# Performance work log

Measured on AMD Instinct MI355X. Metric: run time of the kernel, lower is better.

## Reference

```python
import jax, jax.numpy as jnp
import numpy as np

N_NODES = 50000
N_EDGES = 800000
D = 64        # in_channels == out_channels
EDGE_DIM = 32
H = 8         # num_heads
HD = D // H   # head_dim


def _layer_norm(x, g, b, eps=1e-5):
    m = jnp.mean(x, axis=-1, keepdims=True)
    v = jnp.mean((x - m) ** 2, axis=-1, keepdims=True)
    return (x - m) * jax.lax.rsqrt(v + eps) * g + b


def setup_inputs() -> dict:
    key = jax.random.key(0)
    ks = jax.random.split(key, 20)
    s = 0.05
    inp = {
        'x': jax.random.normal(ks[0], (N_NODES, D), jnp.float32),
        'edge_index': jax.random.randint(ks[1], (2, N_EDGES), 0, N_NODES, dtype=jnp.int64),
        'edge_attr': jax.random.normal(ks[2], (N_EDGES, EDGE_DIM), jnp.float32),
        'Wq': jax.random.normal(ks[3], (D, D), jnp.float32) * s,
        'bq': jnp.zeros((D,), jnp.float32),
        'Wk': jax.random.normal(ks[4], (D, D), jnp.float32) * s,
        'bk': jnp.zeros((D,), jnp.float32),
        'Wv': jax.random.normal(ks[5], (D, D), jnp.float32) * s,
        'bv': jnp.zeros((D,), jnp.float32),
        'We': jax.random.normal(ks[6], (EDGE_DIM, D), jnp.float32) * s,
        'be': jnp.zeros((D,), jnp.float32),
        'Wo': jax.random.normal(ks[7], (D, D), jnp.float32) * s,
        'bo': jnp.zeros((D,), jnp.float32),
        'g1': jnp.ones((D,), jnp.float32),
        'b1': jnp.zeros((D,), jnp.float32),
        'g2': jnp.ones((D,), jnp.float32),
        'b2': jnp.zeros((D,), jnp.float32),
        'Wf1': jax.random.normal(ks[8], (D, 2 * D), jnp.float32) * s,
        'bf1': jnp.zeros((2 * D,), jnp.float32),
        'Wf2': jax.random.normal(ks[9], (2 * D, D), jnp.float32) * s,
        'bf2': jnp.zeros((D,), jnp.float32),
    }
    return inp


def reference(x, edge_index, edge_attr, Wq, bq, Wk, bk, Wv, bv, We, be, Wo, bo,
              g1, b1, g2, b2, Wf1, bf1, Wf2, bf2):
    num_nodes = x.shape[0]
    # add_self_loops with fill_value=0.0
    ar = jnp.arange(num_nodes, dtype=edge_index.dtype)
    src = jnp.concatenate([edge_index[0], ar])
    dst = jnp.concatenate([edge_index[1], ar])
    ea = jnp.concatenate([edge_attr, jnp.zeros((num_nodes, edge_attr.shape[1]), edge_attr.dtype)])

    q = (x @ Wq + bq).reshape(num_nodes, H, HD)
    k = (x @ Wk + bk).reshape(num_nodes, H, HD)
    v = (x @ Wv + bv).reshape(num_nodes, H, HD)
    ee = (ea @ We + be).reshape(-1, H, HD)  # [E', H, HD]

    # gather, score, global softmax over all edges (dim=0, as in source)
    scores = jnp.sum(q[dst] * (k[src] + ee), axis=-1) / (HD ** 0.5)  # [E', H]
    alpha = jax.nn.softmax(scores, axis=0)
    messages = alpha[..., None] * (v[src] + ee)  # [E', H, HD]

    out_sum = jax.ops.segment_sum(messages, dst, num_segments=num_nodes)
    counts = jax.ops.segment_sum(jnp.ones(dst.shape, x.dtype), dst, num_segments=num_nodes)
    counts = jnp.maximum(counts, 1.0)
    out = (out_sum / counts[:, None, None]).reshape(num_nodes, -1)

    h = _layer_norm(x + out @ Wo + bo, g1, b1)
    ffn = jax.nn.gelu(h @ Wf1 + bf1, approximate=False) @ Wf2 + bf2
    # dropout in eval mode -> identity
    return _layer_norm(h + ffn, g2, b2)
```

## Files before the change

kernel.cpp:

```cpp
#include <hip/hip_runtime.h>
#include <hip/hip_bf16.h>
#include <math.h>

#define N_NODES 50000
#define N_EDGES 800000
#define D 64
#define ED 32
#define NB 196

#define Q_OFF    0
#define K8_OFF   1600000
#define V8_OFF   2400000
#define EE_OFF   3200000
#define OS_OFF   16000000
#define S_OFF    17600000
#define RP_OFF   17600016
#define SRCP_OFF 17650018
#define POSE_OFF 18450018
#define DEG_OFF  19250018
#define WOFF_OFF 19300018
#define BSUM_OFF 19350018
#define H_OFF    0
#define F1_OFF   EE_OFF

typedef __bf16 bf16x8 __attribute__((ext_vector_type(8)));
typedef float  f32x4  __attribute__((ext_vector_type(4)));

__device__ __forceinline__ ushort f2bf(float f) {
  uint u = __float_as_uint(f);
  uint r = (u + 0x7FFFu + ((u >> 16) & 1u)) >> 16;
  return (ushort)r;
}
__device__ __forceinline__ float bfu2f(ushort u) {
  return __uint_as_float(((uint)u) << 16);
}
__device__ __forceinline__ void unpack8(uint4 u, float (&f)[8]) {
  f[0] = __uint_as_float(u.x << 16); f[1] = __uint_as_float(u.x & 0xffff0000u);
  f[2] = __uint_as_float(u.y << 16); f[3] = __uint_as_float(u.y & 0xffff0000u);
  f[4] = __uint_as_float(u.z << 16); f[5] = __uint_as_float(u.z & 0xffff0000u);
  f[6] = __uint_as_float(u.w << 16); f[7] = __uint_as_float(u.w & 0xffff0000u);
}
__device__ __forceinline__ void unfp8(uint2 u, float (&f)[8]) {
  f[0] = __builtin_amdgcn_cvt_f32_fp8((int)u.x, 0);
  f[1] = __builtin_amdgcn_cvt_f32_fp8((int)u.x, 1);
  f[2] = __builtin_amdgcn_cvt_f32_fp8((int)u.x, 2);
  f[3] = __builtin_amdgcn_cvt_f32_fp8((int)u.x, 3);
  f[4] = __builtin_amdgcn_cvt_f32_fp8((int)u.y, 0);
  f[5] = __builtin_amdgcn_cvt_f32_fp8((int)u.y, 1);
  f[6] = __builtin_amdgcn_cvt_f32_fp8((int)u.y, 2);
  f[7] = __builtin_amdgcn_cvt_f32_fp8((int)u.y, 3);
}
__device__ __forceinline__ bf16x8 pack_bf8(float4 a, float4 b) {
  bf16x8 r;
  r[0] = (__bf16)a.x; r[1] = (__bf16)a.y; r[2] = (__bf16)a.z; r[3] = (__bf16)a.w;
  r[4] = (__bf16)b.x; r[5] = (__bf16)b.y; r[6] = (__bf16)b.z; r[7] = (__bf16)b.w;
  return r;
}
__device__ __forceinline__ uint pk_fp8(f32x4 acc) {
  uint rr = (uint)__builtin_amdgcn_cvt_pk_fp8_f32(acc[0], acc[1], 0, false);
  return (uint)__builtin_amdgcn_cvt_pk_fp8_f32(acc[2], acc[3], (int)rr, true);
}

__global__ __launch_bounds__(256) void k_qkv_mfma(
    const float* __restrict__ x,
    const float* __restrict__ Wq, const float* __restrict__ bq,
    const float* __restrict__ Wk, const float* __restrict__ bk,
    const float* __restrict__ Wv, const float* __restrict__ bv,
    ushort* __restrict__ q, unsigned char* __restrict__ k8,
    unsigned char* __restrict__ v8,
    int* __restrict__ deg, float* __restrict__ S) {
  const int tid0 = blockIdx.x * 256 + threadIdx.x;
  if (tid0 < N_NODES) deg[tid0] = 0;
  if (tid0 < 16) S[tid0] = 0.f;

  const int lane = threadIdx.x & 63;
  const int wid  = threadIdx.x >> 6;
  const int r  = lane & 15;
  const int kg = lane >> 4;
  const float* Ws[3] = {Wq, Wk, Wv};
  const float* bs[3] = {bq, bk, bv};

  bf16x8 afrag[3][4][2];
  float  bias[3][4][4];
#pragma unroll
  for (int m = 0; m < 3; ++m)
#pragma unroll
    for (int nt = 0; nt < 4; ++nt) {
#pragma unroll
      for (int kk = 0; kk < 2; ++kk)
#pragma unroll
        for (int j = 0; j < 8; ++j)
          afrag[m][nt][kk][j] = (__bf16)Ws[m][(kk * 32 + kg * 8 + j) * 64 + nt * 16 + r];
#pragma unroll
      for (int j = 0; j < 4; ++j) bias[m][nt][j] = bs[m][nt * 16 + kg * 4 + j];
    }

  const int ntile = N_NODES / 16;
  const int nw = gridDim.x * 4;
  for (int t = blockIdx.x * 4 + wid; t < ntile; t += nw) {
    const int base = t * 16;
    const float4* xr = reinterpret_cast<const float4*>(x + (size_t)(base + r) * 64 + kg * 8);
    const bf16x8 xf0 = pack_bf8(xr[0], xr[1]);
    const bf16x8 xf1 = pack_bf8(xr[8], xr[9]);
#pragma unroll
    for (int m = 0; m < 3; ++m) {
#pragma unroll
      for (int nt = 0; nt < 4; ++nt) {
        f32x4 acc = {bias[m][nt][0], bias[m][nt][1], bias[m][nt][2], bias[m][nt][3]};
        acc = __builtin_amdgcn_mfma_f32_16x16x32_bf16(afrag[m][nt][0], xf0, acc, 0, 0, 0);
        acc = __builtin_amdgcn_mfma_f32_16x16x32_bf16(afrag[m][nt][1], xf1, acc, 0, 0, 0);
        if (m == 0) {
          ushort4 pk;
          pk.x = f2bf(acc[0]); pk.y = f2bf(acc[1]); pk.z = f2bf(acc[2]); pk.w = f2bf(acc[3]);
          *reinterpret_cast<ushort4*>(q + (size_t)(base + r) * 64 + nt * 16 + kg * 4) = pk;
        } else {
          unsigned char* dst = (m == 1) ? k8 : v8;
          *reinterpret_cast<uint*>(dst + (size_t)(base + r) * 64 + nt * 16 + kg * 4) = pk_fp8(acc);
        }
      }
    }
  }
}

__global__ __launch_bounds__(256) void k_hist(const int* __restrict__ edst,
                                              int* __restrict__ deg) {
  const int i = blockIdx.x * 256 + threadIdx.x;
  if (i < N_EDGES) atomicAdd(&deg[edst[i]], 1);
}

__global__ __launch_bounds__(256) void k_scan_a(const int* __restrict__ deg,
                                                int* __restrict__ bsum) {
  __shared__ int lds[256];
  const int i = blockIdx.x * 256 + threadIdx.x;
  lds[threadIdx.x] = (i < N_NODES) ? deg[i] : 0;
  __syncthreads();
  for (int s = 128; s > 0; s >>= 1) {
    if (threadIdx.x < s) lds[threadIdx.x] += lds[threadIdx.x + s];
    __syncthreads();
  }
  if (threadIdx.x == 0) bsum[blockIdx.x] = lds[0];
}

__global__ __launch_bounds__(256) void k_scan_c(const int* __restrict__ deg,
                                                const int* __restrict__ bsum,
                                                int* __restrict__ rowptr,
                                                int* __restrict__ woff) {
  __shared__ int lds[256];
  const int t = threadIdx.x;
  lds[t] = (t < blockIdx.x) ? bsum[t] : 0;
  __syncthreads();
  for (int s = 128; s > 0; s >>= 1) {
    if (t < s) lds[t] += lds[t + s];
    __syncthreads();
  }
  const int base0 = lds[0];
  __syncthreads();
  const int i = blockIdx.x * 256 + t;
  const int d = (i < N_NODES) ? deg[i] : 0;
  lds[t] = d;
  __syncthreads();
  for (int off = 1; off < 256; off <<= 1) {
    const int val = (t >= off) ? lds[t - off] : 0;
    __syncthreads();
    lds[t] += val;
    __syncthreads();
  }
  const int ex = base0 + lds[t] - d;
  if (i < N_NODES) { rowptr[i] = ex; woff[i] = ex; }
  if (i == N_NODES - 1) rowptr[N_NODES] = ex + d;
}

__global__ __launch_bounds__(256) void k_scatter(const int* __restrict__ esrc,
                                                 const int* __restrict__ edst,
                                                 int* __restrict__ woff,
                                                 int* __restrict__ srcp,
                                                 int* __restrict__ pose) {
  const int i = blockIdx.x * 256 + threadIdx.x;
  if (i < N_EDGES) {
    const int pos = atomicAdd(&woff[edst[i]], 1);
    srcp[pos] = esrc[i];
    pose[i] = pos;
  }
}

__global__ __launch_bounds__(256) void k_ee_mfma(
    const int* __restrict__ pose, const float* __restrict__ ea,
    const float* __restrict__ We, const float* __restrict__ be,
    unsigned char* __restrict__ ee8) {
  const int lane = threadIdx.x & 63;
  const int wid  = threadIdx.x >> 6;
  const int r  = lane & 15;
  const int kg = lane >> 4;

  bf16x8 afrag[4];
  float  bias[4][4];
#pragma unroll
  for (int nt = 0; nt < 4; ++nt) {
#pragma unroll
    for (int j = 0; j < 8; ++j)
      afrag[nt][j] = (__bf16)We[(kg * 8 + j) * 64 + nt * 16 + r];
#pragma unroll
    for (int j = 0; j < 4; ++j) bias[nt][j] = be[nt * 16 + kg * 4 + j];
  }

  const int ntile = N_EDGES / 16;
  const int nw = gridDim.x * 4;
  for (int t = blockIdx.x * 4 + wid; t < ntile; t += nw) {
    const int base = t * 16;
    const int pos = pose[base + r];
    const float4* ar = reinterpret_cast<const float4*>(ea + (size_t)(base + r) * 32 + kg * 8);
    const bf16x8 bfrag = pack_bf8(ar[0], ar[1]);
#pragma unroll
    for (int nt = 0; nt < 4; ++nt) {
      f32x4 acc = {bias[nt][0], bias[nt][1], bias[nt][2], bias[nt][3]};
      acc = __builtin_amdgcn_mfma_f32_16x16x32_bf16(afrag[nt], bfrag, acc, 0, 0, 0);
      *reinterpret_cast<uint*>(ee8 + (size_t)pos * 64 + nt * 16 + kg * 4) = pk_fp8(acc);
    }
  }
}

__global__ __launch_bounds__(256) void k_gather(
    const int* __restrict__ rowptr, const int* __restrict__ srcp,
    const unsigned char* __restrict__ ee8,
    const ushort* __restrict__ qb, const unsigned char* __restrict__ k8,
    const unsigned char* __restrict__ v8, const float* __restrict__ be,
    ushort* __restrict__ osum, float* __restrict__ S) {
  const int lane = threadIdx.x & 63;
  const int wid  = threadIdx.x >> 6;
  const int h = lane & 7, ei = lane >> 3;
  float bes[8];
#pragma unroll
  for (int i = 0; i < 8; ++i) bes[i] = be[h * 8 + i];
  float sacc = 0.f;
  const int nw = gridDim.x * 4;
  for (int n = blockIdx.x * 4 + wid; n < N_NODES; n += nw) {
    const int beg = rowptr[n], end = rowptr[n + 1];
    float qv[8];
    unpack8(*reinterpret_cast<const uint4*>(qb + (size_t)n * 64 + h * 8), qv);
    float macc[8];
#pragma unroll
    for (int i = 0; i < 8; ++i) macc[i] = 0.f;
    if (ei == 0) {
      float kv[8], vv[8];
      unfp8(*reinterpret_cast<const uint2*>(k8 + (size_t)n * 64 + h * 8), kv);
      unfp8(*reinterpret_cast<const uint2*>(v8 + (size_t)n * 64 + h * 8), vv);
      float sc = 0.f;
#pragma unroll
      for (int i = 0; i < 8; ++i) sc = fmaf(qv[i], kv[i] + bes[i], sc);
      const float w = __expf(sc * 0.3535533905932738f);
      sacc += w;
#pragma unroll
      for (int i = 0; i < 8; ++i) macc[i] = w * (vv[i] + bes[i]);
    }
    int p = beg + ei;
    int src = (p < end) ? srcp[p] : 0;
    for (; p < end; p += 8) {
      const int nsrc = (p + 8 < end) ? srcp[p + 8] : 0;
      float ev[8], kv[8], vv[8];
      unfp8(*reinterpret_cast<const uint2*>(ee8 + (size_t)p * 64 + h * 8), ev);
      unfp8(*reinterpret_cast<const uint2*>(k8 + (size_t)src * 64 + h * 8), kv);
      unfp8(*reinterpret_cast<const uint2*>(v8 + (size_t)src * 64 + h * 8), vv);
      float sc = 0.f;
#pragma unroll
      for (int i = 0; i < 8; ++i) sc = fmaf(qv[i], kv[i] + ev[i], sc);
      const float w = __expf(sc * 0.3535533905932738f);
      sacc += w;
#pragma unroll
      for (int i = 0; i < 8; ++i) macc[i] = fmaf(w, vv[i] + ev[i], macc[i]);
      src = nsrc;
    }
#pragma unroll
    for (int i = 0; i < 8; ++i) {
      macc[i] += __shfl_xor(macc[i], 8);
      macc[i] += __shfl_xor(macc[i], 16);
      macc[i] += __shfl_xor(macc[i], 32);
    }
    if (ei == 0) {
      uint pk[4];
#pragma unroll
      for (int i = 0; i < 4; ++i)
        pk[i] = (uint)f2bf(macc[2 * i]) | ((uint)f2bf(macc[2 * i + 1]) << 16);
      *reinterpret_cast<uint4*>(osum + (size_t)n * 64 + h * 8) =
          make_uint4(pk[0], pk[1], pk[2], pk[3]);
    }
  }
  sacc += __shfl_xor(sacc, 8);
  sacc += __shfl_xor(sacc, 16);
  sacc += __shfl_xor(sacc, 32);
  if (ei == 0) atomicAdd(&S[h], sacc);
}

__global__ __launch_bounds__(256) void k_ln1_mfma(
    const ushort* __restrict__ osum, const int* __restrict__ rowptr,
    const float* __restrict__ S, const float* __restrict__ x,
    const float* __restrict__ Wo, const float* __restrict__ bo,
    const float* __restrict__ g1, const float* __restrict__ b1,
    ushort* __restrict__ h) {
  const int lane = threadIdx.x & 63;
  const int wid  = threadIdx.x >> 6;
  const int r  = lane & 15;
  const int kg = lane >> 4;

  bf16x8 afrag[4][2];
  float bias[4][4], g1f[4][4], b1f[4][4];
#pragma unroll
  for (int nt = 0; nt < 4; ++nt) {
#pragma unroll
    for (int kk = 0; kk < 2; ++kk)
#pragma unroll
      for (int j = 0; j < 8; ++j)
        afrag[nt][kk][j] = (__bf16)Wo[(kk * 32 + kg * 8 + j) * 64 + nt * 16 + r];
#pragma unroll
    for (int j = 0; j < 4; ++j) {
      bias[nt][j] = bo[nt * 16 + kg * 4 + j];
      g1f[nt][j]  = g1[nt * 16 + kg * 4 + j];
      b1f[nt][j]  = b1[nt * 16 + kg * 4 + j];
    }
  }
  float invSv[8];
#pragma unroll
  for (int i = 0; i < 8; ++i) invSv[i] = 1.0f / S[i];

  const int ntile = N_NODES / 16;
  const int nw = gridDim.x * 4;
  for (int t = blockIdx.x * 4 + wid; t < ntile; t += nw) {
    const int node = t * 16 + r;
    const float invc = 1.0f / (float)(rowptr[node + 1] - rowptr[node] + 1);
    bf16x8 bfrag[2];
#pragma unroll
    for (int kk = 0; kk < 2; ++kk) {
      float tmp[8];
      unpack8(*reinterpret_cast<const uint4*>(osum + (size_t)node * 64 + kk * 32 + kg * 8), tmp);
      const float sc = invSv[kk * 4 + kg] * invc;
      bf16x8 bf;
#pragma unroll
      for (int e = 0; e < 8; ++e) bf[e] = (__bf16)(tmp[e] * sc);
      bfrag[kk] = bf;
    }
    float tv[4][4];
    float sum = 0.f;
#pragma unroll
    for (int nt = 0; nt < 4; ++nt) {
      f32x4 acc = {bias[nt][0], bias[nt][1], bias[nt][2], bias[nt][3]};
      acc = __builtin_amdgcn_mfma_f32_16x16x32_bf16(afrag[nt][0], bfrag[0], acc, 0, 0, 0);
      acc = __builtin_amdgcn_mfma_f32_16x16x32_bf16(afrag[nt][1], bfrag[1], acc, 0, 0, 0);
      const float4 xv = *reinterpret_cast<const float4*>(x + (size_t)node * 64 + nt * 16 + kg * 4);
      tv[nt][0] = acc[0] + xv.x; tv[nt][1] = acc[1] + xv.y;
      tv[nt][2] = acc[2] + xv.z; tv[nt][3] = acc[3] + xv.w;
      sum += (tv[nt][0] + tv[nt][1]) + (tv[nt][2] + tv[nt][3]);
    }
    sum += __shfl_xor(sum, 16);
    sum += __shfl_xor(sum, 32);
    const float m = sum * (1.0f / 64.0f);
    float var = 0.f;
#pragma unroll
    for (int nt = 0; nt < 4; ++nt)
#pragma unroll
      for (int j = 0; j < 4; ++j) { const float d = tv[nt][j] - m; var = fmaf(d, d, var); }
    var += __shfl_xor(var, 16);
    var += __shfl_xor(var, 32);
    const float rinv = rsqrtf(var * (1.0f / 64.0f) + 1e-5f);
#pragma unroll
    for (int nt = 0; nt < 4; ++nt) {
      ushort4 pk;
      pk.x = f2bf((tv[nt][0] - m) * rinv * g1f[nt][0] + b1f[nt][0]);
      pk.y = f2bf((tv[nt][1] - m) * rinv * g1f[nt][1] + b1f[nt][1]);
      pk.z = f2bf((tv[nt][2] - m) * rinv * g1f[nt][2] + b1f[nt][2]);
      pk.w = f2bf((tv[nt][3] - m) * rinv * g1f[nt][3] + b1f[nt][3]);
      *reinterpret_cast<ushort4*>(h + (size_t)node * 64 + nt * 16 + kg * 4) = pk;
    }
  }
}

__global__ __launch_bounds__(256) void k_ffn1_mfma(
    const ushort* __restrict__ h, const float* __restrict__ Wf1,
    const float* __restrict__ bf1, ushort* __restrict__ f1) {
  const int lane = threadIdx.x & 63;
  const int wid  = threadIdx.x >> 6;
  const int r  = lane & 15;
  const int kg = lane >> 4;

  bf16x8 afrag[8][2];
  float bias[8][4];
#pragma unroll
  for (int nt = 0; nt < 8; ++nt) {
#pragma unroll
    for (int kk = 0; kk < 2; ++kk)
#pragma unroll
      for (int j = 0; j < 8; ++j)
        afrag[nt][kk][j] = (__bf16)Wf1[(kk * 32 + kg * 8 + j) * 128 + nt * 16 + r];
#pragma unroll
    for (int j = 0; j < 4; ++j) bias[nt][j] = bf1[nt * 16 + kg * 4 + j];
  }

  const int ntile = N_NODES / 16;
  const int nw = gridDim.x * 4;
  for (int t = blockIdx.x * 4 + wid; t < ntile; t += nw) {
    const int node = t * 16 + r;
    const bf16x8 bf0 = *reinterpret_cast<const bf16x8*>(h + (size_t)node * 64 + kg * 8);
    const bf16x8 bf1g = *reinterpret_cast<const bf16x8*>(h + (size_t)node * 64 + 32 + kg * 8);
#pragma unroll
    for (int nt = 0; nt < 8; ++nt) {
      f32x4 acc = {bias[nt][0], bias[nt][1], bias[nt][2], bias[nt][3]};
      acc = __builtin_amdgcn_mfma_f32_16x16x32_bf16(afrag[nt][0], bf0, acc, 0, 0, 0);
      acc = __builtin_amdgcn_mfma_f32_16x16x32_bf16(afrag[nt][1], bf1g, acc, 0, 0, 0);
      ushort4 pk;
      pk.x = f2bf(0.5f * acc[0] * (1.0f + erff(acc[0] * 0.7071067811865475f)));
      pk.y = f2bf(0.5f * acc[1] * (1.0f + erff(acc[1] * 0.7071067811865475f)));
      pk.z = f2bf(0.5f * acc[2] * (1.0f + erff(acc[2] * 0.7071067811865475f)));
      pk.w = f2bf(0.5f * acc[3] * (1.0f + erff(acc[3] * 0.7071067811865475f)));
      *reinterpret_cast<ushort4*>(f1 + (size_t)node * 128 + nt * 16 + kg * 4) = pk;
    }
  }
}

__global__ __launch_bounds__(256) void k_ffn2_mfma(
    const ushort* __restrict__ f1, const ushort* __restrict__ h,
    const float* __restrict__ Wf2, const float* __restrict__ bf2,
    const float* __restrict__ g2, const float* __restrict__ b2,
    float* __restrict__ out) {
  const int lane = threadIdx.x & 63;
  const int wid  = threadIdx.x >> 6;
  const int r  = lane & 15;
  const int kg = lane >> 4;

  bf16x8 afrag[4][4];
  float bias[4][4], g2f[4][4], b2f[4][4];
#pragma unroll
  for (int nt = 0; nt < 4; ++nt) {
#pragma unroll
    for (int kk = 0; kk < 4; ++kk)
#pragma unroll
      for (int j = 0; j < 8; ++j)
        afrag[nt][kk][j] = (__bf16)Wf2[(kk * 32 + kg * 8 + j) * 64 + nt * 16 + r];
#pragma unroll
    for (int j = 0; j < 4; ++j) {
      bias[nt][j] = bf2[nt * 16 + kg * 4 + j];
      g2f[nt][j]  = g2[nt * 16 + kg * 4 + j];
      b2f[nt][j]  = b2[nt * 16 + kg * 4 + j];
    }
  }

  const int ntile = N_NODES / 16;
  const int nw = gridDim.x * 4;
  for (int t = blockIdx.x * 4 + wid; t < ntile; t += nw) {
    const int node = t * 16 + r;
    bf16x8 bfrag[4];
#pragma unroll
    for (int kk = 0; kk < 4; ++kk)
      bfrag[kk] = *reinterpret_cast<const bf16x8*>(f1 + (size_t)node * 128 + kk * 32 + kg * 8);
    float tv[4][4];
    float sum = 0.f;
#pragma unroll
    for (int nt = 0; nt < 4; ++nt) {
      f32x4 acc = {bias[nt][0], bias[nt][1], bias[nt][2], bias[nt][3]};
      acc = __builtin_amdgcn_mfma_f32_16x16x32_bf16(afrag[nt][0], bfrag[0], acc, 0, 0, 0);
      acc = __builtin_amdgcn_mfma_f32_16x16x32_bf16(afrag[nt][1], bfrag[1], acc, 0, 0, 0);
      acc = __builtin_amdgcn_mfma_f32_16x16x32_bf16(afrag[nt][2], bfrag[2], acc, 0, 0, 0);
      acc = __builtin_amdgcn_mfma_f32_16x16x32_bf16(afrag[nt][3], bfrag[3], acc, 0, 0, 0);
      const ushort4 hv = *reinterpret_cast<const ushort4*>(h + (size_t)node * 64 + nt * 16 + kg * 4);
      tv[nt][0] = acc[0] + bfu2f(hv.x); tv[nt][1] = acc[1] + bfu2f(hv.y);
      tv[nt][2] = acc[2] + bfu2f(hv.z); tv[nt][3] = acc[3] + bfu2f(hv.w);
      sum += (tv[nt][0] + tv[nt][1]) + (tv[nt][2] + tv[nt][3]);
    }
    sum += __shfl_xor(sum, 16);
    sum += __shfl_xor(sum, 32);
    const float m = sum * (1.0f / 64.0f);
    float var = 0.f;
#pragma unroll
    for (int nt = 0; nt < 4; ++nt)
#pragma unroll
      for (int j = 0; j < 4; ++j) { const float d = tv[nt][j] - m; var = fmaf(d, d, var); }
    var += __shfl_xor(var, 16);
    var += __shfl_xor(var, 32);
    const float rinv = rsqrtf(var * (1.0f / 64.0f) + 1e-5f);
#pragma unroll
    for (int nt = 0; nt < 4; ++nt) {
      float4 o;
      o.x = (tv[nt][0] - m) * rinv * g2f[nt][0] + b2f[nt][0];
      o.y = (tv[nt][1] - m) * rinv * g2f[nt][1] + b2f[nt][1];
      o.z = (tv[nt][2] - m) * rinv * g2f[nt][2] + b2f[nt][2];
      o.w = (tv[nt][3] - m) * rinv * g2f[nt][3] + b2f[nt][3];
      *reinterpret_cast<float4*>(out + (size_t)node * 64 + nt * 16 + kg * 4) = o;
    }
  }
}

extern "C" void kernel_launch(void* const* d_in, const int* in_sizes, int n_in,
                              void* d_out, int out_size, void* d_ws, size_t ws_size,
                              hipStream_t stream) {
  const float* x    = (const float*)d_in[0];
  const int*   ei   = (const int*)d_in[1];
  const int*   esrc = ei;
  const int*   edst = ei + N_EDGES;
  const float* ea   = (const float*)d_in[2];
  const float* Wq   = (const float*)d_in[3];
  const float* bq   = (const float*)d_in[4];
  const float* Wk   = (const float*)d_in[5];
  const float* bk   = (const float*)d_in[6];
  const float* Wv   = (const float*)d_in[7];
  const float* bv   = (const float*)d_in[8];
  const float* We   = (const float*)d_in[9];
  const float* be   = (const float*)d_in[10];
  const float* Wo   = (const float*)d_in[11];
  const float* bo   = (const float*)d_in[12];
  const float* g1   = (const float*)d_in[13];
  const float* b1   = (const float*)d_in[14];
  const float* g2   = (const float*)d_in[15];
  const float* b2   = (const float*)d_in[16];
  const float* Wf1  = (const float*)d_in[17];
  const float* bf1  = (const float*)d_in[18];
  const float* Wf2  = (const float*)d_in[19];
  const float* bf2  = (const float*)d_in[20];

  float* ws    = (float*)d_ws;
  ushort* q    = (ushort*)(ws + Q_OFF);
  unsigned char* k8  = (unsigned char*)(ws + K8_OFF);
  unsigned char* v8  = (unsigned char*)(ws + V8_OFF);
  unsigned char* ee8 = (unsigned char*)(ws + EE_OFF);
  ushort* osum = (ushort*)(ws + OS_OFF);
  float* S     = ws + S_OFF;
  int*   rowptr = (int*)(ws + RP_OFF);
  int*   srcp   = (int*)(ws + SRCP_OFF);
  int*   pose   = (int*)(ws + POSE_OFF);
  int*   deg    = (int*)(ws + DEG_OFF);
  int*   woff   = (int*)(ws + WOFF_OFF);
  int*   bsum   = (int*)(ws + BSUM_OFF);
  ushort* h    = (ushort*)(ws + H_OFF);
  ushort* f1   = (ushort*)(ws + F1_OFF);
  float* out   = (float*)d_out;

  const dim3 B(256);
  const int edgeBlocks = (N_EDGES + 255) / 256;

  k_qkv_mfma<<<dim3(256), B, 0, stream>>>(x, Wq, bq, Wk, bk, Wv, bv, q, k8, v8, deg, S);
  k_hist<<<dim3(edgeBlocks), B, 0, stream>>>(edst, deg);
  k_scan_a<<<dim3(NB), B, 0, stream>>>(deg, bsum);
  k_scan_c<<<dim3(NB), B, 0, stream>>>(deg, bsum, rowptr, woff);
  k_scatter<<<dim3(edgeBlocks), B, 0, stream>>>(esrc, edst, woff, srcp, pose);
  k_ee_mfma<<<dim3(1024), B, 0, stream>>>(pose, ea, We, be, ee8);
  k_gather<<<dim3(1024), B, 0, stream>>>(rowptr, srcp, ee8, q, k8, v8, be, osum, S);
  k_ln1_mfma<<<dim3(256), B, 0, stream>>>(osum, rowptr, S, x, Wo, bo, g1, b1, h);
  k_ffn1_mfma<<<dim3(256), B, 0, stream>>>(h, Wf1, bf1, f1);
  k_ffn2_mfma<<<dim3(256), B, 0, stream>>>(f1, h, Wf2, bf2, g2, b2, out);
}
```

Before: 269.0 us.

## Split node-centric gather into edge-parallel message kernel and per-node sum

The fused per-node gather is replaced by two kernels. An edge-parallel kernel computes attention weights and weighted messages for every CSR-sorted edge and stores them as fp8, using a new dst-per-position array. A per-node kernel then sums the contiguous messages. The aim is to remove load imbalance from varying node degree and the serial per-node loop latency. In exchange it adds an extra write and read of an 800k×64 fp8 message buffer, another fp8 quantization step on the messages, and one more launch.

New measurement: 397.8 us. 47.8% more time.

```diff
diff --git a/kernel.cpp b/kernel.cpp
--- a/kernel.cpp
+++ b/kernel.cpp
@@ -17,9 +17,11 @@
 #define RP_OFF   17600016
 #define SRCP_OFF 17650018
 #define POSE_OFF 18450018
-#define DEG_OFF  19250018
-#define WOFF_OFF 19300018
-#define BSUM_OFF 19350018
+#define DSTP_OFF 19250018
+#define DEG_OFF  20050018
+#define WOFF_OFF 20100018
+#define BSUM_OFF 20150018
+#define MSG_OFF  20150274
 #define H_OFF    0
 #define F1_OFF   EE_OFF
 
@@ -174,11 +176,14 @@
                                                  const int* __restrict__ edst,
                                                  int* __restrict__ woff,
                                                  int* __restrict__ srcp,
+                                                 int* __restrict__ dstp,
                                                  int* __restrict__ pose) {
   const int i = blockIdx.x * 256 + threadIdx.x;
   if (i < N_EDGES) {
-    const int pos = atomicAdd(&woff[edst[i]], 1);
+    const int d = edst[i];
+    const int pos = atomicAdd(&woff[d], 1);
     srcp[pos] = esrc[i];
+    dstp[pos] = d;
     pose[i] = pos;
   }
 }
@@ -219,9 +224,47 @@
   }
 }
 
-__global__ __launch_bounds__(256) void k_gather(
-    const int* __restrict__ rowptr, const int* __restrict__ srcp,
+__global__ __launch_bounds__(256) void k_edge(
+    const int* __restrict__ srcp, const int* __restrict__ dstp,
     const unsigned char* __restrict__ ee8,
+    const ushort* __restrict__ qb, const unsigned char* __restrict__ k8,
+    const unsigned char* __restrict__ v8,
+    unsigned char* __restrict__ msg8, float* __restrict__ S) {
+  const int lane = threadIdx.x & 63;
+  const int wid  = threadIdx.x >> 6;
+  const int h = lane & 7, ei = lane >> 3;
+  float sacc = 0.f;
+  const int nw = gridDim.x * 4;
+  const int ntrip = N_EDGES / 8;
+  for (int t = blockIdx.x * 4 + wid; t < ntrip; t += nw) {
+    const int p = t * 8 + ei;
+    const int src = srcp[p];
+    const int dst = dstp[p];
+    float qv[8], kv[8], vv[8], ev[8];
+    unpack8(*reinterpret_cast<const uint4*>(qb + (size_t)dst * 64 + h * 8), qv);
+    unfp8(*reinterpret_cast<const uint2*>(k8 + (size_t)src * 64 + h * 8), kv);
+    unfp8(*reinterpret_cast<const uint2*>(v8 + (size_t)src * 64 + h * 8), vv);
+    unfp8(*reinterpret_cast<const uint2*>(ee8 + (size_t)p * 64 + h * 8), ev);
+    float sc = 0.f;
+#pragma unroll
+    for (int i = 0; i < 8; ++i) sc = fmaf(qv[i], kv[i] + ev[i], sc);
+    const float w = __expf(sc * 0.3535533905932738f);
+    sacc += w;
+    f32x4 m0 = {w * (vv[0] + ev[0]), w * (vv[1] + ev[1]),
+                w * (vv[2] + ev[2]), w * (vv[3] + ev[3])};
+    f32x4 m1 = {w * (vv[4] + ev[4]), w * (vv[5] + ev[5]),
+                w * (vv[6] + ev[6]), w * (vv[7] + ev[7])};
+    *reinterpret_cast<uint2*>(msg8 + (size_t)p * 64 + h * 8) =
+        make_uint2(pk_fp8(m0), pk_fp8(m1));
+  }
+  sacc += __shfl_xor(sacc, 8);
+  sacc += __shfl_xor(sacc, 16);
+  sacc += __shfl_xor(sacc, 32);
+  if (ei == 0) atomicAdd(&S[h], sacc);
+}
+
+__global__ __launch_bounds__(256) void k_sum(
+    const int* __restrict__ rowptr, const unsigned char* __restrict__ msg8,
     const ushort* __restrict__ qb, const unsigned char* __restrict__ k8,
     const unsigned char* __restrict__ v8, const float* __restrict__ be,
     ushort* __restrict__ osum, float* __restrict__ S) {
@@ -235,13 +278,12 @@
   const int nw = gridDim.x * 4;
   for (int n = blockIdx.x * 4 + wid; n < N_NODES; n += nw) {
     const int beg = rowptr[n], end = rowptr[n + 1];
-    float qv[8];
-    unpack8(*reinterpret_cast<const uint4*>(qb + (size_t)n * 64 + h * 8), qv);
     float macc[8];
 #pragma unroll
     for (int i = 0; i < 8; ++i) macc[i] = 0.f;
     if (ei == 0) {
-      float kv[8], vv[8];
+      float qv[8], kv[8], vv[8];
+      unpack8(*reinterpret_cast<const uint4*>(qb + (size_t)n * 64 + h * 8), qv);
       unfp8(*reinterpret_cast<const uint2*>(k8 + (size_t)n * 64 + h * 8), kv);
       unfp8(*reinterpret_cast<const uint2*>(v8 + (size_t)n * 64 + h * 8), vv);
       float sc = 0.f;
@@ -252,22 +294,11 @@
 #pragma unroll
       for (int i = 0; i < 8; ++i) macc[i] = w * (vv[i] + bes[i]);
     }
-    int p = beg + ei;
-    int src = (p < end) ? srcp[p] : 0;
-    for (; p < end; p += 8) {
-      const int nsrc = (p + 8 < end) ? srcp[p + 8] : 0;
-      float ev[8], kv[8], vv[8];
-      unfp8(*reinterpret_cast<const uint2*>(ee8 + (size_t)p * 64 + h * 8), ev);
-      unfp8(*reinterpret_cast<const uint2*>(k8 + (size_t)src * 64 + h * 8), kv);
-      unfp8(*reinterpret_cast<const uint2*>(v8 + (size_t)src * 64 + h * 8), vv);
-      float sc = 0.f;
-#pragma unroll
-      for (int i = 0; i < 8; ++i) sc = fmaf(qv[i], kv[i] + ev[i], sc);
-      const float w = __expf(sc * 0.3535533905932738f);
-      sacc += w;
-#pragma unroll
-      for (int i = 0; i < 8; ++i) macc[i] = fmaf(w, vv[i] + ev[i], macc[i]);
-      src = nsrc;
+    for (int p = beg + ei; p < end; p += 8) {
+      float mv[8];
+      unfp8(*reinterpret_cast<const uint2*>(msg8 + (size_t)p * 64 + h * 8), mv);
+#pragma unroll
+      for (int i = 0; i < 8; ++i) macc[i] += mv[i];
     }
 #pragma unroll
     for (int i = 0; i < 8; ++i) {
@@ -523,9 +554,11 @@
   int*   rowptr = (int*)(ws + RP_OFF);
   int*   srcp   = (int*)(ws + SRCP_OFF);
   int*   pose   = (int*)(ws + POSE_OFF);
+  int*   dstp   = (int*)(ws + DSTP_OFF);
   int*   deg    = (int*)(ws + DEG_OFF);
   int*   woff   = (int*)(ws + WOFF_OFF);
   int*   bsum   = (int*)(ws + BSUM_OFF);
+  unsigned char* msg8 = (unsigned char*)(ws + MSG_OFF);
   ushort* h    = (ushort*)(ws + H_OFF);
   ushort* f1   = (ushort*)(ws + F1_OFF);
   float* out   = (float*)d_out;
@@ -537,9 +570,10 @@
   k_hist<<<dim3(edgeBlocks), B, 0, stream>>>(edst, deg);
   k_scan_a<<<dim3(NB), B, 0, stream>>>(deg, bsum);
   k_scan_c<<<dim3(NB), B, 0, stream>>>(deg, bsum, rowptr, woff);
-  k_scatter<<<dim3(edgeBlocks), B, 0, stream>>>(esrc, edst, woff, srcp, pose);
+  k_scatter<<<dim3(edgeBlocks), B, 0, stream>>>(esrc, edst, woff, srcp, dstp, pose);
   k_ee_mfma<<<dim3(1024), B, 0, stream>>>(pose, ea, We, be, ee8);
-  k_gather<<<dim3(1024), B, 0, stream>>>(rowptr, srcp, ee8, q, k8, v8, be, osum, S);
+  k_edge<<<dim3(2048), B, 0, stream>>>(srcp, dstp, ee8, q, k8, v8, msg8, S);
+  k_sum<<<dim3(1024), B, 0, stream>>>(rowptr, msg8, q, k8, v8, be, osum, S);
   k_ln1_mfma<<<dim3(256), B, 0, stream>>>(osum, rowptr, S, x, Wo, bo, g1, b1, h);
   k_ffn1_mfma<<<dim3(256), B, 0, stream>>>(h, Wf1, bf1, f1);
   k_ffn2_mfma<<<dim3(256), B, 0, stream>>>(f1, h, Wf2, bf2, g2, b2, out);
```
